# Kernel optimization log

Measured on AMD Instinct MI355X. Metric: run time of the kernel, lower is better.

The kernel has to match this reference:

```python
import jax, jax.numpy as jnp
import numpy as np

B, S, E, H = 2, 2048, 1024, 16
D = E // H
THETA = 10000.0


def _rope_cos_sin():
    # Faithful to source: freqs_cis is indexed by input_shape[1], which after
    # _split_heads is the HEAD dimension, so 'positions' are head indices 0..H-1.
    freqs = 1.0 / (THETA ** (jnp.arange(0, D, 2, dtype=jnp.float32) / D))  # [D/2]
    pos = jnp.arange(H, dtype=jnp.float32)  # head indices (source bug, reproduced)
    ang = jnp.outer(pos, freqs)  # [H, D/2]
    # broadcast shape [1, H, 1, D/2] against [B, H, S, D/2]
    return jnp.cos(ang)[None, :, None, :], jnp.sin(ang)[None, :, None, :]


def _apply_rope(x, cos, sin):
    # x: [B, H, S, D]; complex pairs are (even, odd) along last dim
    xe, xo = x[..., 0::2], x[..., 1::2]
    re = xe * cos - xo * sin
    im = xe * sin + xo * cos
    # interleave back: view_as_real(...).flatten(3)
    return jnp.stack([re, im], axis=-1).reshape(x.shape)


def setup_inputs() -> dict:
    key = jax.random.key(0)
    ks = jax.random.split(key, 5)
    s = 0.02
    return {
        "hidden_states": jax.random.normal(ks[0], (B, S, E), dtype=jnp.float32),
        "W_attn": jax.random.normal(ks[1], (E, 3 * E), dtype=jnp.float32) * s,
        "b_attn": jnp.zeros((3 * E,), dtype=jnp.float32),
        "W_proj": jax.random.normal(ks[2], (E, E), dtype=jnp.float32) * s,
        "b_proj": jnp.zeros((E,), dtype=jnp.float32),
    }


def reference(hidden_states, W_attn, b_attn, W_proj, b_proj):
    qkv = hidden_states @ W_attn + b_attn  # [B, S, 3E]
    q, k, v = jnp.split(qkv, 3, axis=-1)
    # split heads -> [B, H, S, D]
    def split_heads(t):
        return t.reshape(B, S, H, D).transpose(0, 2, 1, 3)
    q, k, v = split_heads(q), split_heads(k), split_heads(v)
    cos, sin = _rope_cos_sin()
    q = _apply_rope(q, cos, sin)
    k = _apply_rope(k, cos, sin)
    scores = jnp.einsum("bhqd,bhkd->bhqk", q, k) / jnp.sqrt(jnp.float32(D))
    causal = jnp.tril(jnp.ones((S, S), dtype=bool))
    neg = jnp.finfo(scores.dtype).min
    scores = jnp.where(causal[None, None], scores, neg)
    attn = jax.nn.softmax(scores, axis=-1)
    out = jnp.einsum("bhqk,bhkd->bhqd", attn, v)  # [B, H, S, D]
    out = out.transpose(0, 2, 1, 3).reshape(B, S, E)  # merge heads
    return out @ W_proj + b_proj
```

## Files before the change

### kernel.cpp

```cpp
#include <hip/hip_runtime.h>
#include <hip/hip_bf16.h>
#include <cstdint>
#include <cstddef>


typedef float  f32x4 __attribute__((ext_vector_type(4)));
typedef __bf16 bf16x8 __attribute__((ext_vector_type(8)));

__device__ __forceinline__ unsigned short f2bf(float f) {
  union { __bf16 b; unsigned short u; } c; c.b = (__bf16)f; return c.u;
}
__device__ __forceinline__ unsigned short bf2u(__bf16 b) {
  union { __bf16 b; unsigned short u; } c; c.b = b; return c.u;
}

__global__ __launch_bounds__(256) void cast_x_k(const float* __restrict__ in,
                                                __bf16* __restrict__ out) {
  size_t i = (size_t)blockIdx.x * 256 + threadIdx.x;
  f32x4 a = *(const f32x4*)(in + i * 8);
  f32x4 b = *(const f32x4*)(in + i * 8 + 4);
  bf16x8 o;
  o[0]=(__bf16)a[0]; o[1]=(__bf16)a[1]; o[2]=(__bf16)a[2]; o[3]=(__bf16)a[3];
  o[4]=(__bf16)b[0]; o[5]=(__bf16)b[1]; o[6]=(__bf16)b[2]; o[7]=(__bf16)b[3];
  *(bf16x8*)(out + i * 8) = o;
}

template<bool ROPE>
__global__ __launch_bounds__(256) void transpose_rot_k(const float* __restrict__ W,
                                                       __bf16* __restrict__ Wt,
                                                       int Kd, int Nd) {
  __shared__ float tile[32][33];
  const int tx = threadIdx.x, ty = threadIdx.y;
  const int n0 = blockIdx.x * 32, k0 = blockIdx.y * 32;
#pragma unroll
  for (int i = 0; i < 4; i++)
    tile[ty + 8 * i][tx] = W[(size_t)(k0 + ty + 8 * i) * Nd + n0 + tx];
  __syncthreads();
#pragma unroll
  for (int i = 0; i < 4; i++) {
    int nl = ty + 8 * i;
    int n  = n0 + nl;
    float v;
    if (ROPE && n < 2048) {
      int nn = n & 1023;
      int h = nn >> 6, d = nn & 63, ip = d >> 1;
      float ang = (float)h * powf(10000.0f, -(float)ip / 32.0f);
      float s, c; sincosf(ang, &s, &c);
      float xe = tile[tx][nl & ~1], xo = tile[tx][nl | 1];
      v = (d & 1) ? (xe * s + xo * c) : (xe * c - xo * s);
    } else {
      v = tile[tx][nl];
    }
    Wt[(size_t)n * Kd + k0 + tx] = (__bf16)v;
  }
}

__global__ __launch_bounds__(256) void rot_bias_k(const float* __restrict__ b,
                                                  float* __restrict__ out) {
  int n = blockIdx.x * 256 + threadIdx.x;
  if (n < 3072) {
    float v;
    if (n < 2048) {
      int nn = n & 1023, h = nn >> 6, d = nn & 63, ip = d >> 1;
      float ang = (float)h * powf(10000.0f, -(float)ip / 32.0f);
      float s, c; sincosf(ang, &s, &c);
      float xe = b[n & ~1], xo = b[n | 1];
      v = (d & 1) ? (xe * s + xo * c) : (xe * c - xo * s);
    } else v = b[n];
    out[n] = v;
  }
}

template<int MODE>
__global__ __launch_bounds__(256) void gemm_bt_k(
    const __bf16* __restrict__ A, const __bf16* __restrict__ Bt,
    const float* __restrict__ bias, float* __restrict__ outf,
    __bf16* __restrict__ Qo, __bf16* __restrict__ Ko, __bf16* __restrict__ Vo,
    int M, int N, int K)
{
  __shared__ __align__(16) char Asm[8192];
  __shared__ __align__(16) char Bsm[8192];
  const int tid = threadIdx.x;
  const int m0 = blockIdx.y * 128, n0 = blockIdx.x * 128;
  const int wid = tid >> 6, lane = tid & 63;
  const int wr = wid >> 1, wc = wid & 1;
  const int li = lane & 15, gq = lane >> 4;

  const f32x4 fzero = {0.f, 0.f, 0.f, 0.f};
  f32x4 acc[4][4];
#pragma unroll
  for (int i = 0; i < 4; i++)
#pragma unroll
    for (int j = 0; j < 4; j++) acc[i][j] = fzero;

  const int NT = K >> 5;
  const int row0 = tid >> 2, cb = tid & 3;
  const int row1 = row0 + 64;

  f32x4 pa0 = *(const f32x4*)(A  + (size_t)(m0 + row0) * K + cb * 8);
  f32x4 pa1 = *(const f32x4*)(A  + (size_t)(m0 + row1) * K + cb * 8);
  f32x4 pb0 = *(const f32x4*)(Bt + (size_t)(n0 + row0) * K + cb * 8);
  f32x4 pb1 = *(const f32x4*)(Bt + (size_t)(n0 + row1) * K + cb * 8);

  for (int kt = 0; kt < NT; ++kt) {
    __syncthreads();
    *(f32x4*)(Asm + row0 * 64 + cb * 16) = pa0;
    *(f32x4*)(Asm + row1 * 64 + cb * 16) = pa1;
    *(f32x4*)(Bsm + row0 * 64 + cb * 16) = pb0;
    *(f32x4*)(Bsm + row1 * 64 + cb * 16) = pb1;
    __syncthreads();
    if (kt + 1 < NT) {
      int ko = (kt + 1) * 32;
      pa0 = *(const f32x4*)(A  + (size_t)(m0 + row0) * K + ko + cb * 8);
      pa1 = *(const f32x4*)(A  + (size_t)(m0 + row1) * K + ko + cb * 8);
      pb0 = *(const f32x4*)(Bt + (size_t)(n0 + row0) * K + ko + cb * 8);
      pb1 = *(const f32x4*)(Bt + (size_t)(n0 + row1) * K + ko + cb * 8);
    }
    bf16x8 af[4], bfr[4];
#pragma unroll
    for (int mi = 0; mi < 4; mi++)
      af[mi] = *(const bf16x8*)(Asm + (wr * 64 + mi * 16 + li) * 64 + gq * 16);
#pragma unroll
    for (int ni = 0; ni < 4; ni++)
      bfr[ni] = *(const bf16x8*)(Bsm + (wc * 64 + ni * 16 + li) * 64 + gq * 16);
#pragma unroll
    for (int mi = 0; mi < 4; mi++)
#pragma unroll
      for (int ni = 0; ni < 4; ni++)
        acc[mi][ni] = __builtin_amdgcn_mfma_f32_16x16x32_bf16(af[mi], bfr[ni],
                                                              acc[mi][ni], 0, 0, 0);
  }

#pragma unroll
  for (int ni = 0; ni < 4; ni++) {
    const int n = n0 + wc * 64 + ni * 16 + li;
    const float bv = bias[n];
#pragma unroll
    for (int mi = 0; mi < 4; mi++) {
#pragma unroll
      for (int r = 0; r < 4; r++) {
        const int m = m0 + wr * 64 + mi * 16 + 4 * gq + r;
        const float val = acc[mi][ni][r] + bv;
        if (MODE == 0) {
          const int region = n >> 10, nn = n & 1023;
          const int h = nn >> 6, d = nn & 63;
          const int b = m >> 11, s = m & 2047;
          __bf16* dst = (region == 0) ? Qo : (region == 1) ? Ko : Vo;
          dst[(((size_t)(b * 16 + h)) * 2048 + s) * 64 + d] = (__bf16)val;
        } else {
          outf[(size_t)m * N + n] = val;
        }
      }
    }
  }
}

__global__ __launch_bounds__(256) void attn_k(
    const __bf16* __restrict__ Q, const __bf16* __restrict__ K,
    const __bf16* __restrict__ V, __bf16* __restrict__ O)
{
  __shared__ __align__(16) char Ksm[8192];
  __shared__ __align__(16) char Vsm[8192];
  __shared__ __align__(16) char Psm[4][2048];
  const int qt = blockIdx.x, bh = blockIdx.y;
  const int tid = threadIdx.x, wid = tid >> 6, lane = tid & 63;
  const int li = lane & 15, gq = lane >> 4;
  const size_t base = (size_t)bh * 2048 * 64;
  const int iq = qt * 64 + wid * 16 + li;
  const int swz = (li & 7) << 4;
  const f32x4 fzero = {0.f, 0.f, 0.f, 0.f};

  bf16x8 qf[2];
#pragma unroll
  for (int kc = 0; kc < 2; kc++)
    qf[kc] = *(const bf16x8*)(Q + base + (size_t)iq * 64 + kc * 32 + gq * 8);

  f32x4 o[4];
#pragma unroll
  for (int dn = 0; dn < 4; dn++) o[dn] = fzero;
  float mrun = -1e30f, lrun = 0.f;
  char* pw = Psm[wid];

  for (int kt = 0; kt <= qt; ++kt) {
    __syncthreads();
#pragma unroll
    for (int c = 0; c < 2; c++) {
      int idx = tid + 256 * c;
      int row = idx >> 3, cbk = idx & 7;
      f32x4 dv = *(const f32x4*)(K + base + (size_t)(kt * 64 + row) * 64 + cbk * 8);
      *(f32x4*)(Ksm + ((row * 128 + cbk * 16) ^ ((row & 7) << 4))) = dv;
    }
    {
      int kk = (tid >> 3) * 2;
      int d0 = (tid & 7) * 8;
      bf16x8 v0 = *(const bf16x8*)(V + base + (size_t)(kt * 64 + kk) * 64 + d0);
      bf16x8 v1 = *(const bf16x8*)(V + base + (size_t)(kt * 64 + kk + 1) * 64 + d0);
#pragma unroll
      for (int j = 0; j < 8; j++) {
        int d = d0 + j;
        unsigned w = (unsigned)bf2u(v0[j]) | ((unsigned)bf2u(v1[j]) << 16);
        *(unsigned*)(Vsm + ((d * 128 + kk * 2) ^ ((d & 7) << 4))) = w;
      }
    }
    __syncthreads();

    f32x4 s4[4];
#pragma unroll
    for (int f = 0; f < 4; f++) s4[f] = fzero;
#pragma unroll
    for (int kc = 0; kc < 2; kc++) {
#pragma unroll
      for (int f = 0; f < 4; f++) {
        bf16x8 kf = *(const bf16x8*)(Ksm + (((f * 16 + li) * 128 + kc * 64 + gq * 16) ^ swz));
        s4[f] = __builtin_amdgcn_mfma_f32_16x16x32_bf16(kf, qf[kc], s4[f], 0, 0, 0);
      }
    }
    float p[4][4];
    float tmax = -1e30f;
#pragma unroll
    for (int f = 0; f < 4; f++)
#pragma unroll
      for (int r = 0; r < 4; r++) {
        float sv = s4[f][r] * 0.125f;
        int j = kt * 64 + f * 16 + 4 * gq + r;
        if (j > iq) sv = -1e30f;
        p[f][r] = sv;
        tmax = fmaxf(tmax, sv);
      }
    tmax = fmaxf(tmax, __shfl_xor(tmax, 16));
    tmax = fmaxf(tmax, __shfl_xor(tmax, 32));
    float mnew  = fmaxf(mrun, tmax);
    float alpha = __expf(mrun - mnew);
    mrun = mnew;
    float ts = 0.f;
#pragma unroll
    for (int f = 0; f < 4; f++)
#pragma unroll
      for (int r = 0; r < 4; r++) {
        float pv = __expf(p[f][r] - mnew);
        p[f][r] = pv;
        ts += pv;
      }
    ts += __shfl_xor(ts, 16);
    ts += __shfl_xor(ts, 32);
    lrun = lrun * alpha + ts;
#pragma unroll
    for (int r = 0; r < 4; r++) {
      float ar = __shfl(alpha, 4 * gq + r);
#pragma unroll
      for (int dn = 0; dn < 4; dn++) o[dn][r] *= ar;
    }
#pragma unroll
    for (int f = 0; f < 4; f++) {
      unsigned lo = (unsigned)f2bf(p[f][0]) | ((unsigned)f2bf(p[f][1]) << 16);
      unsigned hi = (unsigned)f2bf(p[f][2]) | ((unsigned)f2bf(p[f][3]) << 16);
      uint2 w2; w2.x = lo; w2.y = hi;
      *(uint2*)(pw + ((li * 128 + f * 32 + gq * 8) ^ swz)) = w2;
    }
#pragma unroll
    for (int kc = 0; kc < 2; kc++) {
      bf16x8 paf = *(const bf16x8*)(pw + ((li * 128 + kc * 64 + gq * 16) ^ swz));
#pragma unroll
      for (int dn = 0; dn < 4; dn++) {
        bf16x8 vb = *(const bf16x8*)(Vsm + (((dn * 16 + li) * 128 + kc * 64 + gq * 16) ^ swz));
        o[dn] = __builtin_amdgcn_mfma_f32_16x16x32_bf16(paf, vb, o[dn], 0, 0, 0);
      }
    }
  }

  const int b = bh >> 4, h = bh & 15;
#pragma unroll
  for (int r = 0; r < 4; r++) {
    float lr  = __shfl(lrun, 4 * gq + r);
    float inv = 1.0f / lr;
    int qrow = qt * 64 + wid * 16 + 4 * gq + r;
#pragma unroll
    for (int dn = 0; dn < 4; dn++) {
      O[((size_t)(b * 2048 + qrow)) * 1024 + h * 64 + dn * 16 + li] =
          (__bf16)(o[dn][r] * inv);
    }
  }
}

extern "C" void kernel_launch(void* const* d_in, const int* in_sizes, int n_in,
                              void* d_out, int out_size, void* d_ws, size_t ws_size,
                              hipStream_t stream) {
  const float* hidden = (const float*)d_in[0];
  const float* W_attn = (const float*)d_in[1];
  const float* b_attn = (const float*)d_in[2];
  const float* W_proj = (const float*)d_in[3];
  const float* b_proj = (const float*)d_in[4];
  float* out = (float*)d_out;

  char* ws = (char*)d_ws;
  size_t off = 0;
  auto alloc = [&](size_t bytes) -> char* {
    char* p = ws + off;
    off += (bytes + 255) & ~(size_t)255;
    return p;
  };
  __bf16* Xb  = (__bf16*)alloc((size_t)4096 * 1024 * 2);
  __bf16* Wat = (__bf16*)alloc((size_t)3072 * 1024 * 2);
  __bf16* Wpt = (__bf16*)alloc((size_t)1024 * 1024 * 2);
  float*  ba  = (float*) alloc((size_t)3072 * 4);
  __bf16* Qb  = (__bf16*)alloc((size_t)32 * 2048 * 64 * 2);
  __bf16* Kb  = (__bf16*)alloc((size_t)32 * 2048 * 64 * 2);
  __bf16* Vb  = (__bf16*)alloc((size_t)32 * 2048 * 64 * 2);
  __bf16* Ob  = (__bf16*)alloc((size_t)4096 * 1024 * 2);

  cast_x_k<<<2048, 256, 0, stream>>>(hidden, Xb);
  transpose_rot_k<true ><<<dim3(96, 32), dim3(32, 8), 0, stream>>>(W_attn, Wat, 1024, 3072);
  transpose_rot_k<false><<<dim3(32, 32), dim3(32, 8), 0, stream>>>(W_proj, Wpt, 1024, 1024);
  rot_bias_k<<<12, 256, 0, stream>>>(b_attn, ba);

  gemm_bt_k<0><<<dim3(24, 32), 256, 0, stream>>>(Xb, Wat, ba, nullptr,
                                                 Qb, Kb, Vb, 4096, 3072, 1024);
  attn_k<<<dim3(32, 32), 256, 0, stream>>>(Qb, Kb, Vb, Ob);
  gemm_bt_k<1><<<dim3(8, 32), 256, 0, stream>>>(Ob, Wpt, b_proj, out,
                                                nullptr, nullptr, nullptr,
                                                4096, 1024, 1024);
}
```

Measured before the change: 261.6 us.

## Use direct global-to-LDS loads in GEMM and double-buffer a larger attention block

The GEMM drops its register-staged prefetch and loads A/B tiles straight into LDS with global_load_lds, which removes register traffic but loses the overlap of the next tile's load with the current MFMA work. The attention kernel now uses 512 threads covering 128 query rows per block. K and V tiles are double-buffered in LDS, and separate warp groups load K and V for the next tile while the current one is computed. Warps skip key tiles that lie entirely in their causal-masked region. This halves the grid and adds LDS use, which may reduce occupancy and leave per-block causal work less balanced.

```diff
diff --git a/kernel.cpp b/kernel.cpp
--- a/kernel.cpp
+++ b/kernel.cpp
@@ -12,6 +12,12 @@
 }
 __device__ __forceinline__ unsigned short bf2u(__bf16 b) {
   union { __bf16 b; unsigned short u; } c; c.b = b; return c.u;
+}
+
+__device__ __forceinline__ void gload_lds16(const void* g, void* l) {
+  __builtin_amdgcn_global_load_lds(
+      (const __attribute__((address_space(1))) unsigned int*)g,
+      (__attribute__((address_space(3))) unsigned int*)l, 16, 0, 0);
 }
 
 __global__ __launch_bounds__(256) void cast_x_k(const float* __restrict__ in,
@@ -94,28 +100,19 @@
     for (int j = 0; j < 4; j++) acc[i][j] = fzero;
 
   const int NT = K >> 5;
-  const int row0 = tid >> 2, cb = tid & 3;
-  const int row1 = row0 + 64;
-
-  f32x4 pa0 = *(const f32x4*)(A  + (size_t)(m0 + row0) * K + cb * 8);
-  f32x4 pa1 = *(const f32x4*)(A  + (size_t)(m0 + row1) * K + cb * 8);
-  f32x4 pb0 = *(const f32x4*)(Bt + (size_t)(n0 + row0) * K + cb * 8);
-  f32x4 pb1 = *(const f32x4*)(Bt + (size_t)(n0 + row1) * K + cb * 8);
 
   for (int kt = 0; kt < NT; ++kt) {
+    const int ko = kt * 32;
+#pragma unroll
+    for (int it = 0; it < 2; it++) {
+      const int idx = wid * 128 + it * 64 + lane;
+      const int row = idx >> 2, cb = idx & 3;
+      char* la = Asm + (size_t)(wid * 128 + it * 64) * 16;
+      char* lb = Bsm + (size_t)(wid * 128 + it * 64) * 16;
+      gload_lds16(A  + (size_t)(m0 + row) * K + ko + cb * 8, la);
+      gload_lds16(Bt + (size_t)(n0 + row) * K + ko + cb * 8, lb);
+    }
     __syncthreads();
-    *(f32x4*)(Asm + row0 * 64 + cb * 16) = pa0;
-    *(f32x4*)(Asm + row1 * 64 + cb * 16) = pa1;
-    *(f32x4*)(Bsm + row0 * 64 + cb * 16) = pb0;
-    *(f32x4*)(Bsm + row1 * 64 + cb * 16) = pb1;
-    __syncthreads();
-    if (kt + 1 < NT) {
-      int ko = (kt + 1) * 32;
-      pa0 = *(const f32x4*)(A  + (size_t)(m0 + row0) * K + ko + cb * 8);
-      pa1 = *(const f32x4*)(A  + (size_t)(m0 + row1) * K + ko + cb * 8);
-      pb0 = *(const f32x4*)(Bt + (size_t)(n0 + row0) * K + ko + cb * 8);
-      pb1 = *(const f32x4*)(Bt + (size_t)(n0 + row1) * K + ko + cb * 8);
-    }
     bf16x8 af[4], bfr[4];
 #pragma unroll
     for (int mi = 0; mi < 4; mi++)
@@ -129,6 +126,7 @@
       for (int ni = 0; ni < 4; ni++)
         acc[mi][ni] = __builtin_amdgcn_mfma_f32_16x16x32_bf16(af[mi], bfr[ni],
                                                               acc[mi][ni], 0, 0, 0);
+    __syncthreads();
   }
 
 #pragma unroll
@@ -155,20 +153,22 @@
   }
 }
 
-__global__ __launch_bounds__(256) void attn_k(
+__global__ __launch_bounds__(512) void attn_k(
     const __bf16* __restrict__ Q, const __bf16* __restrict__ K,
     const __bf16* __restrict__ V, __bf16* __restrict__ O)
 {
-  __shared__ __align__(16) char Ksm[8192];
-  __shared__ __align__(16) char Vsm[8192];
-  __shared__ __align__(16) char Psm[4][2048];
+  __shared__ __align__(16) char Ksm[2][8192];
+  __shared__ __align__(16) char Vsm[2][8192];
+  __shared__ __align__(16) char Psm[8][2048];
   const int qt = blockIdx.x, bh = blockIdx.y;
   const int tid = threadIdx.x, wid = tid >> 6, lane = tid & 63;
   const int li = lane & 15, gq = lane >> 4;
   const size_t base = (size_t)bh * 2048 * 64;
-  const int iq = qt * 64 + wid * 16 + li;
+  const int iq = qt * 128 + wid * 16 + li;
+  const int wkmax = qt * 128 + wid * 16 + 15;
   const int swz = (li & 7) << 4;
   const f32x4 fzero = {0.f, 0.f, 0.f, 0.f};
+  const int ktmax = 2 * qt + 1;
 
   bf16x8 qf[2];
 #pragma unroll
@@ -181,90 +181,117 @@
   float mrun = -1e30f, lrun = 0.f;
   char* pw = Psm[wid];
 
-  for (int kt = 0; kt <= qt; ++kt) {
-    __syncthreads();
-#pragma unroll
-    for (int c = 0; c < 2; c++) {
-      int idx = tid + 256 * c;
-      int row = idx >> 3, cbk = idx & 7;
-      f32x4 dv = *(const f32x4*)(K + base + (size_t)(kt * 64 + row) * 64 + cbk * 8);
-      *(f32x4*)(Ksm + ((row * 128 + cbk * 16) ^ ((row & 7) << 4))) = dv;
-    }
-    {
-      int kk = (tid >> 3) * 2;
-      int d0 = (tid & 7) * 8;
-      bf16x8 v0 = *(const bf16x8*)(V + base + (size_t)(kt * 64 + kk) * 64 + d0);
-      bf16x8 v1 = *(const bf16x8*)(V + base + (size_t)(kt * 64 + kk + 1) * 64 + d0);
+  const bool roleK = (wid < 4);
+  const int st = tid & 255;
+  const int krow0 = st >> 3, kcb = st & 7;
+  const int krow1 = krow0 + 32;
+  const int vkk = (st >> 3) * 2, vd0 = (st & 7) * 8;
+  f32x4 kreg0, kreg1;
+  bf16x8 vreg0, vreg1;
+
+  auto loadTile = [&](int kt) {
+    if (roleK) {
+      kreg0 = *(const f32x4*)(K + base + (size_t)(kt * 64 + krow0) * 64 + kcb * 8);
+      kreg1 = *(const f32x4*)(K + base + (size_t)(kt * 64 + krow1) * 64 + kcb * 8);
+    } else {
+      vreg0 = *(const bf16x8*)(V + base + (size_t)(kt * 64 + vkk)     * 64 + vd0);
+      vreg1 = *(const bf16x8*)(V + base + (size_t)(kt * 64 + vkk + 1) * 64 + vd0);
+    }
+  };
+  auto writeTile = [&](int buf) {
+    if (roleK) {
+      *(f32x4*)(Ksm[buf] + ((krow0 * 128 + kcb * 16) ^ ((krow0 & 7) << 4))) = kreg0;
+      *(f32x4*)(Ksm[buf] + ((krow1 * 128 + kcb * 16) ^ ((krow1 & 7) << 4))) = kreg1;
+    } else {
 #pragma unroll
       for (int j = 0; j < 8; j++) {
-        int d = d0 + j;
-        unsigned w = (unsigned)bf2u(v0[j]) | ((unsigned)bf2u(v1[j]) << 16);
-        *(unsigned*)(Vsm + ((d * 128 + kk * 2) ^ ((d & 7) << 4))) = w;
-      }
-    }
-    __syncthreads();
-
-    f32x4 s4[4];
-#pragma unroll
-    for (int f = 0; f < 4; f++) s4[f] = fzero;
-#pragma unroll
-    for (int kc = 0; kc < 2; kc++) {
+        int d = vd0 + j;
+        unsigned w = (unsigned)bf2u(vreg0[j]) | ((unsigned)bf2u(vreg1[j]) << 16);
+        *(unsigned*)(Vsm[buf] + ((d * 128 + vkk * 2) ^ ((d & 7) << 4))) = w;
+      }
+    }
+  };
+
+  loadTile(0);
+  writeTile(0);
+  __syncthreads();
+  int cur = 0;
+
+  for (int kt = 0; kt <= ktmax; ++kt) {
+    if (kt < ktmax) loadTile(kt + 1);
+
+    if (kt * 64 <= wkmax) {
+      f32x4 s4[4];
+#pragma unroll
+      for (int f = 0; f < 4; f++) s4[f] = fzero;
+#pragma unroll
+      for (int kc = 0; kc < 2; kc++) {
+#pragma unroll
+        for (int f = 0; f < 4; f++) {
+          bf16x8 kf = *(const bf16x8*)(Ksm[cur] +
+              (((f * 16 + li) * 128 + kc * 64 + gq * 16) ^ swz));
+          s4[f] = __builtin_amdgcn_mfma_f32_16x16x32_bf16(kf, qf[kc], s4[f], 0, 0, 0);
+        }
+      }
+      float p[4][4];
+      float tmax = -1e30f;
+#pragma unroll
+      for (int f = 0; f < 4; f++)
+#pragma unroll
+        for (int r = 0; r < 4; r++) {
+          float sv = s4[f][r] * 0.125f;
+          int j = kt * 64 + f * 16 + 4 * gq + r;
+          if (j > iq) sv = -1e30f;
+          p[f][r] = sv;
+          tmax = fmaxf(tmax, sv);
+        }
+      tmax = fmaxf(tmax, __shfl_xor(tmax, 16));
+      tmax = fmaxf(tmax, __shfl_xor(tmax, 32));
+      float mnew  = fmaxf(mrun, tmax);
+      float alpha = __expf(mrun - mnew);
+      mrun = mnew;
+      float ts = 0.f;
+#pragma unroll
+      for (int f = 0; f < 4; f++)
+#pragma unroll
+        for (int r = 0; r < 4; r++) {
+          float pv = __expf(p[f][r] - mnew);
+          p[f][r] = pv;
+          ts += pv;
+        }
+      ts += __shfl_xor(ts, 16);
+      ts += __shfl_xor(ts, 32);
+      lrun = lrun * alpha + ts;
+#pragma unroll
+      for (int r = 0; r < 4; r++) {
+        float ar = __shfl(alpha, 4 * gq + r);
+#pragma unroll
+        for (int dn = 0; dn < 4; dn++) o[dn][r] *= ar;
+      }
 #pragma unroll
       for (int f = 0; f < 4; f++) {
-        bf16x8 kf = *(const bf16x8*)(Ksm + (((f * 16 + li) * 128 + kc * 64 + gq * 16) ^ swz));
-        s4[f] = __builtin_amdgcn_mfma_f32_16x16x32_bf16(kf, qf[kc], s4[f], 0, 0, 0);
-      }
-    }
-    float p[4][4];
-    float tmax = -1e30f;
-#pragma unroll
-    for (int f = 0; f < 4; f++)
-#pragma unroll
-      for (int r = 0; r < 4; r++) {
-        float sv = s4[f][r] * 0.125f;
-        int j = kt * 64 + f * 16 + 4 * gq + r;
-        if (j > iq) sv = -1e30f;
-        p[f][r] = sv;
-        tmax = fmaxf(tmax, sv);
-      }
-    tmax = fmaxf(tmax, __shfl_xor(tmax, 16));
-    tmax = fmaxf(tmax, __shfl_xor(tmax, 32));
-    float mnew  = fmaxf(mrun, tmax);
-    float alpha = __expf(mrun - mnew);
-    mrun = mnew;
-    float ts = 0.f;
-#pragma unroll
-    for (int f = 0; f < 4; f++)
-#pragma unroll
-      for (int r = 0; r < 4; r++) {
-        float pv = __expf(p[f][r] - mnew);
-        p[f][r] = pv;
-        ts += pv;
-      }
-    ts += __shfl_xor(ts, 16);
-    ts += __shfl_xor(ts, 32);
-    lrun = lrun * alpha + ts;
-#pragma unroll
-    for (int r = 0; r < 4; r++) {
-      float ar = __shfl(alpha, 4 * gq + r);
-#pragma unroll
-      for (int dn = 0; dn < 4; dn++) o[dn][r] *= ar;
-    }
-#pragma unroll
-    for (int f = 0; f < 4; f++) {
-      unsigned lo = (unsigned)f2bf(p[f][0]) | ((unsigned)f2bf(p[f][1]) << 16);
-      unsigned hi = (unsigned)f2bf(p[f][2]) | ((unsigned)f2bf(p[f][3]) << 16);
-      uint2 w2; w2.x = lo; w2.y = hi;
-      *(uint2*)(pw + ((li * 128 + f * 32 + gq * 8) ^ swz)) = w2;
-    }
-#pragma unroll
-    for (int kc = 0; kc < 2; kc++) {
-      bf16x8 paf = *(const bf16x8*)(pw + ((li * 128 + kc * 64 + gq * 16) ^ swz));
-#pragma unroll
-      for (int dn = 0; dn < 4; dn++) {
-        bf16x8 vb = *(const bf16x8*)(Vsm + (((dn * 16 + li) * 128 + kc * 64 + gq * 16) ^ swz));
-        o[dn] = __builtin_amdgcn_mfma_f32_16x16x32_bf16(paf, vb, o[dn], 0, 0, 0);
-      }
+        unsigned lo = (unsigned)f2bf(p[f][0]) | ((unsigned)f2bf(p[f][1]) << 16);
+        unsigned hi = (unsigned)f2bf(p[f][2]) | ((unsigned)f2bf(p[f][3]) << 16);
+        uint2 w2; w2.x = lo; w2.y = hi;
+        *(uint2*)(pw + ((li * 128 + f * 32 + gq * 8) ^ swz)) = w2;
+      }
+#pragma unroll
+      for (int kc = 0; kc < 2; kc++) {
+        bf16x8 paf = *(const bf16x8*)(pw + ((li * 128 + kc * 64 + gq * 16) ^ swz));
+#pragma unroll
+        for (int dn = 0; dn < 4; dn++) {
+          bf16x8 vb = *(const bf16x8*)(Vsm[cur] +
+              (((dn * 16 + li) * 128 + kc * 64 + gq * 16) ^ swz));
+          o[dn] = __builtin_amdgcn_mfma_f32_16x16x32_bf16(paf, vb, o[dn], 0, 0, 0);
+        }
+      }
+    }
+
+    if (kt < ktmax) {
+      __syncthreads();
+      writeTile(cur ^ 1);
+      __syncthreads();
+      cur ^= 1;
     }
   }
 
@@ -273,7 +300,7 @@
   for (int r = 0; r < 4; r++) {
     float lr  = __shfl(lrun, 4 * gq + r);
     float inv = 1.0f / lr;
-    int qrow = qt * 64 + wid * 16 + 4 * gq + r;
+    int qrow = qt * 128 + wid * 16 + 4 * gq + r;
 #pragma unroll
     for (int dn = 0; dn < 4; dn++) {
       O[((size_t)(b * 2048 + qrow)) * 1024 + h * 64 + dn * 16 + li] =
@@ -315,7 +342,7 @@
 
   gemm_bt_k<0><<<dim3(24, 32), 256, 0, stream>>>(Xb, Wat, ba, nullptr,
                                                  Qb, Kb, Vb, 4096, 3072, 1024);
-  attn_k<<<dim3(32, 32), 256, 0, stream>>>(Qb, Kb, Vb, Ob);
+  attn_k<<<dim3(16, 32), 512, 0, stream>>>(Qb, Kb, Vb, Ob);
   gemm_bt_k<1><<<dim3(8, 32), 256, 0, stream>>>(Ob, Wpt, b_proj, out,
                                                 nullptr, nullptr, nullptr,
                                                 4096, 1024, 1024);
```

Result: faster. 249.7 us (-4.6%).
